# Kernel tuning notes

Hardware: AMD Instinct MI355X
Metric: run time of the kernel (lower is better)

Reference implementation:

```python
import jax, jax.numpy as jnp
import numpy as np

H, NHEADS, DK, DV, DFF, MAXLEN = 128, 2, 96, 96, 2048, 43
VIN, VOUT = 32000, 10000
N, T = 256, 43


def layer_norm(x, g, b, eps=1e-5):
    m = jnp.mean(x, axis=-1, keepdims=True)
    v = jnp.mean(jnp.square(x - m), axis=-1, keepdims=True)
    return (x - m) / jnp.sqrt(v + eps) * g + b


def setup_inputs() -> dict:
    key = jax.random.key(0)
    ks = jax.random.split(key, 24)
    def rn(k, shape, scale=0.02):
        return jax.random.normal(k, shape, dtype=jnp.float32) * scale
    return {
        "inputs": jax.random.randint(ks[0], (N, T), 0, VIN),
        "emb": rn(ks[1], (VIN, H)),
        "pos": rn(ks[2], (MAXLEN, H)),
        "Wq": rn(ks[3], (NHEADS, H, DK), 0.05),
        "bq": jnp.zeros((NHEADS, DK), jnp.float32),
        "Wk": rn(ks[4], (NHEADS, H, DK), 0.05),
        "bk": jnp.zeros((NHEADS, DK), jnp.float32),
        "Wv": rn(ks[5], (NHEADS, H, DV), 0.05),
        "bv": jnp.zeros((NHEADS, DV), jnp.float32),
        "Wo": rn(ks[6], (NHEADS * DV, H), 0.05),
        "bo": jnp.zeros((H,), jnp.float32),
        "ln1_g": jnp.ones((H,), jnp.float32),
        "ln1_b": jnp.zeros((H,), jnp.float32),
        "W1": rn(ks[7], (H, DFF), 0.05),
        "b1": jnp.zeros((DFF,), jnp.float32),
        "W2": rn(ks[8], (DFF, H), 0.05),
        "b2": jnp.zeros((H,), jnp.float32),
        "ln2_g": jnp.ones((H,), jnp.float32),
        "ln2_b": jnp.zeros((H,), jnp.float32),
        "Wout": rn(ks[9], (H, VOUT), 0.05),
        "bout": jnp.zeros((VOUT,), jnp.float32),
    }


def reference(inputs, emb, pos, Wq, bq, Wk, bk, Wv, bv, Wo, bo,
              ln1_g, ln1_b, W1, b1, W2, b2, ln2_g, ln2_b, Wout, bout):
    Tcur = inputs.shape[1]
    # embed: token + positional, (N,T,H)
    x = emb[inputs] + pos[:Tcur]
    # multi-head attention (all heads batched on axis 'a')
    q = jnp.einsum("nth,ahk->natk", x, Wq) + bq[:, None, :]
    k = jnp.einsum("nth,ahk->natk", x, Wk) + bk[:, None, :]
    v = jnp.einsum("nth,ahv->natv", x, Wv) + bv[:, None, :]
    scores = jnp.einsum("natk,nask->nats", q, k) / jnp.sqrt(jnp.float32(DK))
    # NOTE: original mask (float-embeddings != pad_idx) is a numerical no-op; omitted.
    probs = jax.nn.softmax(scores, axis=-1)
    att = jnp.einsum("nats,nasv->natv", probs, v)          # (N,A,T,DV)
    multi = att.transpose(0, 2, 1, 3).reshape(att.shape[0], Tcur, NHEADS * DV)
    attn_out = multi @ Wo + bo
    x1 = layer_norm(x + attn_out, ln1_g, ln1_b)
    # feedforward + residual + LN
    ff = jax.nn.relu(x1 @ W1 + b1) @ W2 + b2
    x2 = layer_norm(x1 + ff, ln2_g, ln2_b)
    # final vocab projection (N,T,VOUT)
    return x2 @ Wout + bout
```

## Files before the change

### kernel.cpp

```cpp
#include <hip/hip_runtime.h>
#include <hip/hip_bf16.h>

#define H 128
#define NHEADS 2
#define DK 96
#define DV 96
#define DFF 2048
#define VOUT 10000
#define VOUT_PAD 10112
#define NB 256
#define TT 43
#define NT (NB * TT)
#define MD (NHEADS * DV)
#define MDP 256
#define QKVC 640

typedef short short8v __attribute__((ext_vector_type(8)));
typedef unsigned short ushort8v __attribute__((ext_vector_type(8)));
typedef float f32x4 __attribute__((ext_vector_type(4)));

__device__ __forceinline__ unsigned short f2bf(float f) {
    unsigned b = __float_as_uint(f);
    unsigned r = b + 0x7FFFu + ((b >> 16) & 1u);
    return (unsigned short)(r >> 16);
}
__device__ __forceinline__ float bf2f(unsigned short u) {
    return __uint_as_float((unsigned)u << 16);
}

__global__ __launch_bounds__(256) void embed_kernel(
    const int* __restrict__ inputs, const float* __restrict__ emb,
    const float* __restrict__ pos, float* __restrict__ x,
    unsigned short* __restrict__ xb) {
    int i = blockIdx.x * 256 + threadIdx.x;
    int h = i & (H - 1);
    int nt = i >> 7;
    int t = nt % TT;
    float v = emb[inputs[nt] * H + h] + pos[t * H + h];
    x[i] = v;
    xb[i] = f2bf(v);
}

__global__ __launch_bounds__(256) void wqkv_pack_kernel(
    const float* __restrict__ Wq, const float* __restrict__ bq,
    const float* __restrict__ Wk, const float* __restrict__ bk,
    const float* __restrict__ Wv, const float* __restrict__ bv,
    unsigned short* __restrict__ Wt, float* __restrict__ bias) {
    int row = blockIdx.x * 256 + threadIdx.x;
    if (row >= QKVC) return;
    unsigned short* dst = Wt + (size_t)row * H;
    if (row < 576) {
        int seg = row / 96;
        int d = row - seg * 96;
        int which = seg >> 1;
        int head = seg & 1;
        const float* W  = (which == 0) ? Wq : (which == 1) ? Wk : Wv;
        const float* bi = (which == 0) ? bq : (which == 1) ? bk : bv;
        for (int h = 0; h < H; ++h) dst[h] = f2bf(W[((size_t)head * H + h) * DK + d]);
        bias[row] = bi[head * DK + d];
    } else {
        for (int h = 0; h < H; ++h) dst[h] = 0;
        bias[row] = 0.f;
    }
}

__global__ __launch_bounds__(256) void w1t_kernel(
    const float* __restrict__ W1, unsigned short* __restrict__ W1tb) {
    int n = blockIdx.x * 256 + threadIdx.x;
    ushort8v* dst = (ushort8v*)(W1tb + (size_t)n * H);
    #pragma unroll
    for (int k16 = 0; k16 < 16; ++k16) {
        ushort8v v;
        #pragma unroll
        for (int j = 0; j < 8; ++j)
            v[j] = f2bf(W1[(size_t)(k16 * 8 + j) * DFF + n]);
        dst[k16] = v;
    }
}

__global__ __launch_bounds__(256) void w2t_kernel(
    const float* __restrict__ W2, unsigned short* __restrict__ W2tb) {
    int c = blockIdx.x;
    int j = threadIdx.x;
    for (int k = j; k < DFF; k += 256)
        W2tb[(size_t)c * DFF + k] = f2bf(W2[(size_t)k * H + c]);
}

__global__ __launch_bounds__(256) void wotb_kernel(
    const float* __restrict__ Wo, unsigned short* __restrict__ Wot) {
    int idx = blockIdx.x * 256 + threadIdx.x;
    int c = idx >> 8, k = idx & 255;
    Wot[(size_t)c * MDP + k] = (k < MD) ? f2bf(Wo[(size_t)k * H + c]) : (unsigned short)0;
}

__global__ __launch_bounds__(256) void qkv_mfma_kernel(
    const unsigned short* __restrict__ xb, const unsigned short* __restrict__ Wt,
    const float* __restrict__ bias, unsigned short* __restrict__ qkvb) {
    __shared__ __align__(16) unsigned short As[128][128];
    __shared__ __align__(16) unsigned short Bt[128][128];
    int tid = threadIdx.x;
    int n0 = blockIdx.x * 128;
    int m0 = blockIdx.y * 128;
    {
        const ushort8v* A8 = (const ushort8v*)(xb + (size_t)m0 * H);
        for (int qc = tid; qc < 2048; qc += 256) {
            int row = qc >> 4, o = qc & 15;
            int po = (o & 8) | ((o ^ row) & 7);
            *(ushort8v*)&As[row][po * 8] = A8[qc];
        }
    }
    {
        const ushort8v* B8 = (const ushort8v*)(Wt + (size_t)n0 * H);
        for (int qc = tid; qc < 2048; qc += 256) {
            int row = qc >> 4, o = qc & 15;
            int po = (o & 8) | ((o ^ row) & 7);
            *(ushort8v*)&Bt[row][po * 8] = B8[qc];
        }
    }
    __syncthreads();
    int lane = tid & 63;
    int w = tid >> 6;
    int wr = w >> 1, wc = w & 1;
    int rl = lane & 15, quad = lane >> 4;
    f32x4 acc[4][4];
    #pragma unroll
    for (int i = 0; i < 4; ++i)
        #pragma unroll
        for (int j = 0; j < 4; ++j) acc[i][j] = (f32x4){0.f, 0.f, 0.f, 0.f};
    #pragma unroll
    for (int kk = 0; kk < 4; ++kk) {
        int o = kk * 4 + quad;
        short8v a[4], b[4];
        #pragma unroll
        for (int mi = 0; mi < 4; ++mi) {
            int row = wr * 64 + mi * 16 + rl;
            int po = (o & 8) | ((o ^ row) & 7);
            a[mi] = *(const short8v*)&As[row][po * 8];
        }
        #pragma unroll
        for (int ni = 0; ni < 4; ++ni) {
            int cc = wc * 64 + ni * 16 + rl;
            int po = (o & 8) | ((o ^ cc) & 7);
            b[ni] = *(const short8v*)&Bt[cc][po * 8];
        }
        #pragma unroll
        for (int mi = 0; mi < 4; ++mi)
            #pragma unroll
            for (int ni = 0; ni < 4; ++ni)
                acc[mi][ni] = __builtin_amdgcn_mfma_f32_16x16x32_bf16(
                    a[mi], b[ni], acc[mi][ni], 0, 0, 0);
    }
    #pragma unroll
    for (int ni = 0; ni < 4; ++ni) {
        int col = n0 + wc * 64 + ni * 16 + rl;
        float bv = bias[col];
        #pragma unroll
        for (int mi = 0; mi < 4; ++mi) {
            int rbase = m0 + wr * 64 + mi * 16 + quad * 4;
            #pragma unroll
            for (int r = 0; r < 4; ++r)
                qkvb[(size_t)(rbase + r) * QKVC + col] = f2bf(acc[mi][ni][r] + bv);
        }
    }
}

__global__ __launch_bounds__(256) void attn_core_kernel(
    const unsigned short* __restrict__ qkvb, unsigned short* __restrict__ multi_b) {
    int blk = blockIdx.x;
    int n = blk / NHEADS, a = blk % NHEADS;
    int tid = threadIdx.x;
    __shared__ float qs[TT][DK];
    __shared__ float ks2[TT][DK];
    __shared__ float vs[TT][DV];
    __shared__ float ss[TT][TT + 1];
    for (int i = tid; i < TT * 12 * 3; i += 256) {
        int which = i / (TT * 12);
        int rem = i - which * (TT * 12);
        int t = rem / 12, c8 = rem - t * 12;
        ushort8v u = *(const ushort8v*)(qkvb + (size_t)(n * TT + t) * QKVC
                                        + a * DK + which * 192 + c8 * 8);
        float* dst = ((which == 0) ? &qs[t][0] : (which == 1) ? &ks2[t][0] : &vs[t][0]) + c8 * 8;
        #pragma unroll
        for (int j = 0; j < 8; ++j) dst[j] = bf2f(u[j]);
    }
    __syncthreads();
    const float scale = rsqrtf((float)DK);
    for (int o = tid; o < TT * TT; o += 256) {
        int t = o / TT, s = o - t * TT;
        float acc = 0.f;
        #pragma unroll 8
        for (int d = 0; d < DK; ++d) acc += qs[t][d] * ks2[s][d];
        ss[t][s] = acc * scale;
    }
    __syncthreads();
    if (tid < TT) {
        float m = -1e30f;
        for (int s = 0; s < TT; ++s) m = fmaxf(m, ss[tid][s]);
        float sum = 0.f;
        for (int s = 0; s < TT; ++s) { float e = __expf(ss[tid][s] - m); ss[tid][s] = e; sum += e; }
        float inv = 1.0f / sum;
        for (int s = 0; s < TT; ++s) ss[tid][s] *= inv;
    }
    __syncthreads();
    for (int o = tid; o < TT * DV; o += 256) {
        int t = o / DV, d = o - t * DV;
        float acc = 0.f;
        #pragma unroll 8
        for (int s = 0; s < TT; ++s) acc += ss[t][s] * vs[s][d];
        multi_b[(size_t)(n * TT + t) * MDP + a * DV + d] = f2bf(acc);
    }
}

__global__ __launch_bounds__(256) void woln1_mfma_kernel(
    const unsigned short* __restrict__ mb, const unsigned short* __restrict__ Wot,
    const float* __restrict__ bo, const float* __restrict__ x,
    const float* __restrict__ g, const float* __restrict__ bln,
    float* __restrict__ x1, unsigned short* __restrict__ x1b) {
    __shared__ __align__(16) unsigned short As[128][128];
    __shared__ __align__(16) unsigned short Bt[128][128];
    int tid = threadIdx.x;
    int m0 = blockIdx.x * 128;
    int lane = tid & 63;
    int w = tid >> 6;
    int wr = w >> 1, wc = w & 1;
    int rl = lane & 15, quad = lane >> 4;
    f32x4 acc[4][4];
    #pragma unroll
    for (int i = 0; i < 4; ++i)
        #pragma unroll
        for (int j = 0; j < 4; ++j) acc[i][j] = (f32x4){0.f, 0.f, 0.f, 0.f};
    for (int kc = 0; kc < 2; ++kc) {
        for (int qc = tid; qc < 2048; qc += 256) {
            int row = qc >> 4, o = qc & 15;
            ushort8v v = *(const ushort8v*)(mb + (size_t)(m0 + row) * MDP + kc * 128 + o * 8);
            int po = (o & 8) | ((o ^ row) & 7);
            *(ushort8v*)&As[row][po * 8] = v;
        }
        for (int qc = tid; qc < 2048; qc += 256) {
            int row = qc >> 4, o = qc & 15;
            ushort8v v = *(const ushort8v*)(Wot + (size_t)row * MDP + kc * 128 + o * 8);
            int po = (o & 8) | ((o ^ row) & 7);
            *(ushort8v*)&Bt[row][po * 8] = v;
        }
        __syncthreads();
        #pragma unroll
        for (int kk = 0; kk < 4; ++kk) {
            int o = kk * 4 + quad;
            short8v a[4], b[4];
            #pragma unroll
            for (int mi = 0; mi < 4; ++mi) {
                int row = wr * 64 + mi * 16 + rl;
                int po = (o & 8) | ((o ^ row) & 7);
                a[mi] = *(const short8v*)&As[row][po * 8];
            }
            #pragma unroll
            for (int ni = 0; ni < 4; ++ni) {
                int cc = wc * 64 + ni * 16 + rl;
                int po = (o & 8) | ((o ^ cc) & 7);
                b[ni] = *(const short8v*)&Bt[cc][po * 8];
            }
            #pragma unroll
            for (int mi = 0; mi < 4; ++mi)
                #pragma unroll
                for (int ni = 0; ni < 4; ++ni)
                    acc[mi][ni] = __builtin_amdgcn_mfma_f32_16x16x32_bf16(
                        a[mi], b[ni], acc[mi][ni], 0, 0, 0);
        }
        __syncthreads();
    }
    float gg[4], bb[4], bov[4];
    #pragma unroll
    for (int ni = 0; ni < 4; ++ni) {
        int col = wc * 64 + ni * 16 + rl;
        gg[ni] = g[col]; bb[ni] = bln[col]; bov[ni] = bo[col];
    }
    float sy[4][4], sy2[4][4];
    #pragma unroll
    for (int mi = 0; mi < 4; ++mi)
        #pragma unroll
        for (int r = 0; r < 4; ++r) { sy[mi][r] = 0.f; sy2[mi][r] = 0.f; }
    #pragma unroll
    for (int mi = 0; mi < 4; ++mi) {
        #pragma unroll
        for (int r = 0; r < 4; ++r) {
            int row = wr * 64 + mi * 16 + quad * 4 + r;
            #pragma unroll
            for (int ni = 0; ni < 4; ++ni) {
                int col = wc * 64 + ni * 16 + rl;
                float y = acc[mi][ni][r] + bov[ni] + x[(size_t)(m0 + row) * H + col];
                acc[mi][ni][r] = y;
                sy[mi][r] += y;
                sy2[mi][r] += y * y;
            }
        }
    }
    #pragma unroll
    for (int mi = 0; mi < 4; ++mi)
        #pragma unroll
        for (int r = 0; r < 4; ++r) {
            #pragma unroll
            for (int m = 1; m < 16; m <<= 1) {
                sy[mi][r]  += __shfl_xor(sy[mi][r],  m);
                sy2[mi][r] += __shfl_xor(sy2[mi][r], m);
            }
        }
    float* scr = (float*)&As[0][0];
    if (rl == 0) {
        #pragma unroll
        for (int mi = 0; mi < 4; ++mi)
            #pragma unroll
            for (int r = 0; r < 4; ++r) {
                int row = wr * 64 + mi * 16 + quad * 4 + r;
                scr[wc * 128 + row]       = sy[mi][r];
                scr[256 + wc * 128 + row] = sy2[mi][r];
            }
    }
    __syncthreads();
    #pragma unroll
    for (int mi = 0; mi < 4; ++mi) {
        #pragma unroll
        for (int r = 0; r < 4; ++r) {
            int row = wr * 64 + mi * 16 + quad * 4 + r;
            float tsy  = scr[row] + scr[128 + row];
            float tsy2 = scr[256 + row] + scr[384 + row];
            float mean = tsy * (1.0f / H);
            float var  = tsy2 * (1.0f / H) - mean * mean;
            float rstd = rsqrtf(var + 1e-5f);
            #pragma unroll
            for (int ni = 0; ni < 4; ++ni) {
                int col = wc * 64 + ni * 16 + rl;
                float v = (acc[mi][ni][r] - mean) * rstd * gg[ni] + bb[ni];
                size_t idx = (size_t)(m0 + row) * H + col;
                x1[idx] = v;
                x1b[idx] = f2bf(v);
            }
        }
    }
}

__global__ __launch_bounds__(256) void ffh_kernel(
    const unsigned short* __restrict__ x1b, const unsigned short* __restrict__ W1tb,
    const float* __restrict__ b1, unsigned short* __restrict__ hb) {
    __shared__ __align__(16) unsigned short As[128][128];
    __shared__ __align__(16) unsigned short Bt[128][128];
    int tid = threadIdx.x;
    int n0 = blockIdx.x * 128;
    int m0 = blockIdx.y * 128;
    {
        const ushort8v* A8 = (const ushort8v*)(x1b + (size_t)m0 * H);
        for (int qc = tid; qc < 2048; qc += 256) {
            int row = qc >> 4, o = qc & 15;
            int po = (o & 8) | ((o ^ row) & 7);
            *(ushort8v*)&As[row][po * 8] = A8[qc];
        }
    }
    {
        const ushort8v* B8 = (const ushort8v*)(W1tb + (size_t)n0 * H);
        for (int qc = tid; qc < 2048; qc += 256) {
            int row = qc >> 4, o = qc & 15;
            int po = (o & 8) | ((o ^ row) & 7);
            *(ushort8v*)&Bt[row][po * 8] = B8[qc];
        }
    }
    __syncthreads();
    int lane = tid & 63;
    int w = tid >> 6;
    int wr = w >> 1, wc = w & 1;
    int rl = lane & 15, quad = lane >> 4;
    f32x4 acc[4][4];
    #pragma unroll
    for (int i = 0; i < 4; ++i)
        #pragma unroll
        for (int j = 0; j < 4; ++j) acc[i][j] = (f32x4){0.f, 0.f, 0.f, 0.f};
    #pragma unroll
    for (int kk = 0; kk < 4; ++kk) {
        int o = kk * 4 + quad;
        short8v a[4], b[4];
        #pragma unroll
        for (int mi = 0; mi < 4; ++mi) {
            int row = wr * 64 + mi * 16 + rl;
            int po = (o & 8) | ((o ^ row) & 7);
            a[mi] = *(const short8v*)&As[row][po * 8];
        }
        #pragma unroll
        for (int ni = 0; ni < 4; ++ni) {
            int cc = wc * 64 + ni * 16 + rl;
            int po = (o & 8) | ((o ^ cc) & 7);
            b[ni] = *(const short8v*)&Bt[cc][po * 8];
        }
        #pragma unroll
        for (int mi = 0; mi < 4; ++mi)
            #pragma unroll
            for (int ni = 0; ni < 4; ++ni)
                acc[mi][ni] = __builtin_amdgcn_mfma_f32_16x16x32_bf16(
                    a[mi], b[ni], acc[mi][ni], 0, 0, 0);
    }
    #pragma unroll
    for (int ni = 0; ni < 4; ++ni) {
        int col = n0 + wc * 64 + ni * 16 + rl;
        float bv = b1[col];
        #pragma unroll
        for (int mi = 0; mi < 4; ++mi) {
            int rbase = m0 + wr * 64 + mi * 16 + quad * 4;
            #pragma unroll
            for (int r = 0; r < 4; ++r)
                hb[(size_t)(rbase + r) * DFF + col] =
                    f2bf(fmaxf(acc[mi][ni][r] + bv, 0.f));
        }
    }
}

__global__ __launch_bounds__(256) void ff2_ln2_kernel(
    const unsigned short* __restrict__ hb, const unsigned short* __restrict__ W2tb,
    const float* __restrict__ b2, const float* __restrict__ x1,
    const float* __restrict__ g, const float* __restrict__ bln,
    unsigned short* __restrict__ x2b) {
    __shared__ __align__(16) unsigned short As[128][128];
    __shared__ __align__(16) unsigned short Bt[128][128];
    int tid = threadIdx.x;
    int m0 = blockIdx.x * 128;
    int lane = tid & 63;
    int w = tid >> 6;
    int wr = w >> 1, wc = w & 1;
    int rl = lane & 15, quad = lane >> 4;
    f32x4 acc[4][4];
    #pragma unroll
    for (int i = 0; i < 4; ++i)
        #pragma unroll
        for (int j = 0; j < 4; ++j) acc[i][j] = (f32x4){0.f, 0.f, 0.f, 0.f};
    for (int kc = 0; kc < 16; ++kc) {
        for (int qc = tid; qc < 2048; qc += 256) {
            int row = qc >> 4, o = qc & 15;
            ushort8v v = *(const ushort8v*)(hb + (size_t)(m0 + row) * DFF + kc * 128 + o * 8);
            int po = (o & 8) | ((o ^ row) & 7);
            *(ushort8v*)&As[row][po * 8] = v;
        }
        for (int qc = tid; qc < 2048; qc += 256) {
            int row = qc >> 4, o = qc & 15;
            ushort8v v = *(const ushort8v*)(W2tb + (size_t)row * DFF + kc * 128 + o * 8);
            int po = (o & 8) | ((o ^ row) & 7);
            *(ushort8v*)&Bt[row][po * 8] = v;
        }
        __syncthreads();
        #pragma unroll
        for (int kk = 0; kk < 4; ++kk) {
            int o = kk * 4 + quad;
            short8v a[4], b[4];
            #pragma unroll
            for (int mi = 0; mi < 4; ++mi) {
                int row = wr * 64 + mi * 16 + rl;
                int po = (o & 8) | ((o ^ row) & 7);
                a[mi] = *(const short8v*)&As[row][po * 8];
            }
            #pragma unroll
            for (int ni = 0; ni < 4; ++ni) {
                int cc = wc * 64 + ni * 16 + rl;
                int po = (o & 8) | ((o ^ cc) & 7);
                b[ni] = *(const short8v*)&Bt[cc][po * 8];
            }
            #pragma unroll
            for (int mi = 0; mi < 4; ++mi)
                #pragma unroll
                for (int ni = 0; ni < 4; ++ni)
                    acc[mi][ni] = __builtin_amdgcn_mfma_f32_16x16x32_bf16(
                        a[mi], b[ni], acc[mi][ni], 0, 0, 0);
        }
        __syncthreads();
    }
    float gg[4], bb[4], bov[4];
    #pragma unroll
    for (int ni = 0; ni < 4; ++ni) {
        int col = wc * 64 + ni * 16 + rl;
        gg[ni] = g[col]; bb[ni] = bln[col]; bov[ni] = b2[col];
    }
    float sy[4][4], sy2[4][4];
    #pragma unroll
    for (int mi = 0; mi < 4; ++mi)
        #pragma unroll
        for (int r = 0; r < 4; ++r) { sy[mi][r] = 0.f; sy2[mi][r] = 0.f; }
    #pragma unroll
    for (int mi = 0; mi < 4; ++mi) {
        #pragma unroll
        for (int r = 0; r < 4; ++r) {
            int row = wr * 64 + mi * 16 + quad * 4 + r;
            #pragma unroll
            for (int ni = 0; ni < 4; ++ni) {
                int col = wc * 64 + ni * 16 + rl;
                float y = acc[mi][ni][r] + bov[ni] + x1[(size_t)(m0 + row) * H + col];
                acc[mi][ni][r] = y;
                sy[mi][r] += y;
                sy2[mi][r] += y * y;
            }
        }
    }
    #pragma unroll
    for (int mi = 0; mi < 4; ++mi)
        #pragma unroll
        for (int r = 0; r < 4; ++r) {
            #pragma unroll
            for (int m = 1; m < 16; m <<= 1) {
                sy[mi][r]  += __shfl_xor(sy[mi][r],  m);
                sy2[mi][r] += __shfl_xor(sy2[mi][r], m);
            }
        }
    float* scr = (float*)&As[0][0];
    if (rl == 0) {
        #pragma unroll
        for (int mi = 0; mi < 4; ++mi)
            #pragma unroll
            for (int r = 0; r < 4; ++r) {
                int row = wr * 64 + mi * 16 + quad * 4 + r;
                scr[wc * 128 + row]       = sy[mi][r];
                scr[256 + wc * 128 + row] = sy2[mi][r];
            }
    }
    __syncthreads();
    #pragma unroll
    for (int mi = 0; mi < 4; ++mi) {
        #pragma unroll
        for (int r = 0; r < 4; ++r) {
            int row = wr * 64 + mi * 16 + quad * 4 + r;
            float tsy  = scr[row] + scr[128 + row];
            float tsy2 = scr[256 + row] + scr[384 + row];
            float mean = tsy * (1.0f / H);
            float var  = tsy2 * (1.0f / H) - mean * mean;
            float rstd = rsqrtf(var + 1e-5f);
            #pragma unroll
            for (int ni = 0; ni < 4; ++ni) {
                int col = wc * 64 + ni * 16 + rl;
                x2b[(size_t)(m0 + row) * H + col] =
                    f2bf((acc[mi][ni][r] - mean) * rstd * gg[ni] + bb[ni]);
            }
        }
    }
}

__global__ __launch_bounds__(256) void wtr_kernel(
    const float* __restrict__ W, unsigned short* __restrict__ Wt) {
    int n = blockIdx.x * 256 + threadIdx.x;
    if (n >= VOUT_PAD) return;
    ushort8v* dst = (ushort8v*)(Wt + (size_t)n * H);
    if (n < VOUT) {
        #pragma unroll
        for (int k16 = 0; k16 < 16; ++k16) {
            ushort8v v;
            #pragma unroll
            for (int j = 0; j < 8; ++j)
                v[j] = f2bf(W[(size_t)(k16 * 8 + j) * VOUT + n]);
            dst[k16] = v;
        }
    } else {
        ushort8v z = {};
        #pragma unroll
        for (int k16 = 0; k16 < 16; ++k16) dst[k16] = z;
    }
}

__global__ __launch_bounds__(256) void out_gemm_mfma_kernel(
    const unsigned short* __restrict__ A, const unsigned short* __restrict__ Wt,
    const float* __restrict__ bias, float* __restrict__ C) {
    __shared__ __align__(16) unsigned short As[128][128];
    __shared__ __align__(16) unsigned short Bt[128][128];
    int tid = threadIdx.x;
    int n0 = blockIdx.x * 128;
    int lane = tid & 63;
    int w = tid >> 6;
    int wr = w >> 1, wc = w & 1;
    int rl = lane & 15, quad = lane >> 4;
    {
        const ushort8v* B8 = (const ushort8v*)(Wt + (size_t)n0 * H);
        for (int qc = tid; qc < 2048; qc += 256) {
            int row = qc >> 4, o = qc & 15;
            int po = (o & 8) | ((o ^ row) & 7);
            *(ushort8v*)&Bt[row][po * 8] = B8[qc];
        }
    }
    float bv[4];
    #pragma unroll
    for (int ni = 0; ni < 4; ++ni) {
        int col = n0 + wc * 64 + ni * 16 + rl;
        bv[ni] = (col < VOUT) ? bias[col] : 0.f;
    }
    for (int half = 0; half < 2; ++half) {
        int m0 = (blockIdx.y * 2 + half) * 128;
        {
            const ushort8v* A8 = (const ushort8v*)(A + (size_t)m0 * H);
            for (int qc = tid; qc < 2048; qc += 256) {
                int row = qc >> 4, o = qc & 15;
                int po = (o & 8) | ((o ^ row) & 7);
                *(ushort8v*)&As[row][po * 8] = A8[qc];
            }
        }
        __syncthreads();
        f32x4 acc[4][4];
        #pragma unroll
        for (int i = 0; i < 4; ++i)
            #pragma unroll
            for (int j = 0; j < 4; ++j) acc[i][j] = (f32x4){0.f, 0.f, 0.f, 0.f};
        #pragma unroll
        for (int kk = 0; kk < 4; ++kk) {
            int o = kk * 4 + quad;
            short8v a[4], b[4];
            #pragma unroll
            for (int mi = 0; mi < 4; ++mi) {
                int row = wr * 64 + mi * 16 + rl;
                int po = (o & 8) | ((o ^ row) & 7);
                a[mi] = *(const short8v*)&As[row][po * 8];
            }
            #pragma unroll
            for (int ni = 0; ni < 4; ++ni) {
                int cc = wc * 64 + ni * 16 + rl;
                int po = (o & 8) | ((o ^ cc) & 7);
                b[ni] = *(const short8v*)&Bt[cc][po * 8];
            }
            #pragma unroll
            for (int mi = 0; mi < 4; ++mi)
                #pragma unroll
                for (int ni = 0; ni < 4; ++ni)
                    acc[mi][ni] = __builtin_amdgcn_mfma_f32_16x16x32_bf16(
                        a[mi], b[ni], acc[mi][ni], 0, 0, 0);
        }
        __syncthreads();
        #pragma unroll
        for (int ni = 0; ni < 4; ++ni) {
            int col = n0 + wc * 64 + ni * 16 + rl;
            if (col >= VOUT) continue;
            #pragma unroll
            for (int mi = 0; mi < 4; ++mi) {
                int rbase = m0 + wr * 64 + mi * 16 + quad * 4;
                #pragma unroll
                for (int r = 0; r < 4; ++r)
                    C[(size_t)(rbase + r) * VOUT + col] = acc[mi][ni][r] + bv[ni];
            }
        }
    }
}

extern "C" void kernel_launch(void* const* d_in, const int* in_sizes, int n_in,
                              void* d_out, int out_size, void* d_ws, size_t ws_size,
                              hipStream_t stream) {
    const int*   inputs = (const int*)  d_in[0];
    const float* emb    = (const float*)d_in[1];
    const float* pos    = (const float*)d_in[2];
    const float* Wq     = (const float*)d_in[3];
    const float* bq     = (const float*)d_in[4];
    const float* Wk     = (const float*)d_in[5];
    const float* bk     = (const float*)d_in[6];
    const float* Wv     = (const float*)d_in[7];
    const float* bv     = (const float*)d_in[8];
    const float* Wo     = (const float*)d_in[9];
    const float* bo     = (const float*)d_in[10];
    const float* ln1g   = (const float*)d_in[11];
    const float* ln1b   = (const float*)d_in[12];
    const float* W1     = (const float*)d_in[13];
    const float* b1     = (const float*)d_in[14];
    const float* W2     = (const float*)d_in[15];
    const float* b2     = (const float*)d_in[16];
    const float* ln2g   = (const float*)d_in[17];
    const float* ln2b   = (const float*)d_in[18];
    const float* Wout   = (const float*)d_in[19];
    const float* bout   = (const float*)d_in[20];
    float* out = (float*)d_out;

    float* ws = (float*)d_ws;
    float* x      = ws;
    float* x1     = x + (size_t)NT * H;
    float* bqkv   = x1 + (size_t)NT * H;
    unsigned short* xb      = (unsigned short*)(bqkv + QKVC);
    unsigned short* x1b     = xb + (size_t)NT * H;
    unsigned short* multi_b = x1b + (size_t)NT * H;
    unsigned short* x2b     = multi_b + (size_t)NT * MDP;
    unsigned short* Woutb   = x2b + (size_t)NT * H;
    unsigned short* Wqkvb   = Woutb + (size_t)VOUT_PAD * H;
    unsigned short* W1tb    = Wqkvb + (size_t)QKVC * H;
    unsigned short* W2tb    = W1tb + (size_t)DFF * H;
    unsigned short* Wotb    = W2tb + (size_t)H * DFF;
    unsigned short* qkvb    = Wotb + (size_t)H * MDP;
    unsigned short* hb      = qkvb + (size_t)NT * QKVC;

    wqkv_pack_kernel<<<(QKVC + 255) / 256, 256, 0, stream>>>(
        Wq, bq, Wk, bk, Wv, bv, Wqkvb, bqkv);
    wotb_kernel<<<H * MDP / 256, 256, 0, stream>>>(Wo, Wotb);
    w1t_kernel<<<DFF / 256, 256, 0, stream>>>(W1, W1tb);
    w2t_kernel<<<H, 256, 0, stream>>>(W2, W2tb);
    wtr_kernel<<<(VOUT_PAD + 255) / 256, 256, 0, stream>>>(Wout, Woutb);
    embed_kernel<<<NT * H / 256, 256, 0, stream>>>(inputs, emb, pos, x, xb);
    dim3 gqkv(QKVC / 128, NT / 128);
    qkv_mfma_kernel<<<gqkv, 256, 0, stream>>>(xb, Wqkvb, bqkv, qkvb);
    attn_core_kernel<<<NB * NHEADS, 256, 0, stream>>>(qkvb, multi_b);
    woln1_mfma_kernel<<<NT / 128, 256, 0, stream>>>(multi_b, Wotb, bo, x, ln1g, ln1b, x1, x1b);
    dim3 gff(DFF / 128, NT / 128);
    ffh_kernel<<<gff, 256, 0, stream>>>(x1b, W1tb, b1, hb);
    ff2_ln2_kernel<<<NT / 128, 256, 0, stream>>>(hb, W2tb, b2, x1, ln2g, ln2b, x2b);
    dim3 g5(VOUT_PAD / 128, NT / 256);
    out_gemm_mfma_kernel<<<g5, 256, 0, stream>>>(x2b, Woutb, bout, out);
}
```

Baseline: 724.6 us.

## Split FF2 GEMM over K into four partial slices with separate reduce+LN2 kernel

The second feed-forward GEMM previously ran only NT/128 = 86 blocks, each looping over all of K=2048, which leaves most CUs of the GPU idle. It is now split into four K slices (344 blocks) that write fp32 partial sums to a workspace. A new kernel adds the partials, bias and residual and applies LayerNorm 2 per row. This costs extra global traffic for the four fp32 partial buffers and one more kernel launch.

```diff
diff --git a/kernel.cpp b/kernel.cpp
--- a/kernel.cpp
+++ b/kernel.cpp
@@ -410,15 +410,14 @@
     }
 }
 
-__global__ __launch_bounds__(256) void ff2_ln2_kernel(
+__global__ __launch_bounds__(256) void ff2_splitk_kernel(
     const unsigned short* __restrict__ hb, const unsigned short* __restrict__ W2tb,
-    const float* __restrict__ b2, const float* __restrict__ x1,
-    const float* __restrict__ g, const float* __restrict__ bln,
-    unsigned short* __restrict__ x2b) {
+    float* __restrict__ pws) {
     __shared__ __align__(16) unsigned short As[128][128];
     __shared__ __align__(16) unsigned short Bt[128][128];
     int tid = threadIdx.x;
     int m0 = blockIdx.x * 128;
+    int ks = blockIdx.y;
     int lane = tid & 63;
     int w = tid >> 6;
     int wr = w >> 1, wc = w & 1;
@@ -428,7 +427,8 @@
     for (int i = 0; i < 4; ++i)
         #pragma unroll
         for (int j = 0; j < 4; ++j) acc[i][j] = (f32x4){0.f, 0.f, 0.f, 0.f};
-    for (int kc = 0; kc < 16; ++kc) {
+    for (int kci = 0; kci < 4; ++kci) {
+        int kc = ks * 4 + kci;
         for (int qc = tid; qc < 2048; qc += 256) {
             int row = qc >> 4, o = qc & 15;
             ushort8v v = *(const ushort8v*)(hb + (size_t)(m0 + row) * DFF + kc * 128 + o * 8);
@@ -467,71 +467,62 @@
         }
         __syncthreads();
     }
-    float gg[4], bb[4], bov[4];
     #pragma unroll
     for (int ni = 0; ni < 4; ++ni) {
         int col = wc * 64 + ni * 16 + rl;
-        gg[ni] = g[col]; bb[ni] = bln[col]; bov[ni] = b2[col];
-    }
-    float sy[4][4], sy2[4][4];
-    #pragma unroll
-    for (int mi = 0; mi < 4; ++mi)
-        #pragma unroll
-        for (int r = 0; r < 4; ++r) { sy[mi][r] = 0.f; sy2[mi][r] = 0.f; }
-    #pragma unroll
-    for (int mi = 0; mi < 4; ++mi) {
-        #pragma unroll
-        for (int r = 0; r < 4; ++r) {
-            int row = wr * 64 + mi * 16 + quad * 4 + r;
-            #pragma unroll
-            for (int ni = 0; ni < 4; ++ni) {
-                int col = wc * 64 + ni * 16 + rl;
-                float y = acc[mi][ni][r] + bov[ni] + x1[(size_t)(m0 + row) * H + col];
-                acc[mi][ni][r] = y;
-                sy[mi][r] += y;
-                sy2[mi][r] += y * y;
-            }
-        }
-    }
-    #pragma unroll
-    for (int mi = 0; mi < 4; ++mi)
-        #pragma unroll
-        for (int r = 0; r < 4; ++r) {
-            #pragma unroll
-            for (int m = 1; m < 16; m <<= 1) {
-                sy[mi][r]  += __shfl_xor(sy[mi][r],  m);
-                sy2[mi][r] += __shfl_xor(sy2[mi][r], m);
-            }
-        }
-    float* scr = (float*)&As[0][0];
-    if (rl == 0) {
-        #pragma unroll
-        for (int mi = 0; mi < 4; ++mi)
-            #pragma unroll
-            for (int r = 0; r < 4; ++r) {
-                int row = wr * 64 + mi * 16 + quad * 4 + r;
-                scr[wc * 128 + row]       = sy[mi][r];
-                scr[256 + wc * 128 + row] = sy2[mi][r];
-            }
-    }
-    __syncthreads();
-    #pragma unroll
-    for (int mi = 0; mi < 4; ++mi) {
-        #pragma unroll
-        for (int r = 0; r < 4; ++r) {
-            int row = wr * 64 + mi * 16 + quad * 4 + r;
-            float tsy  = scr[row] + scr[128 + row];
-            float tsy2 = scr[256 + row] + scr[384 + row];
-            float mean = tsy * (1.0f / H);
-            float var  = tsy2 * (1.0f / H) - mean * mean;
-            float rstd = rsqrtf(var + 1e-5f);
-            #pragma unroll
-            for (int ni = 0; ni < 4; ++ni) {
-                int col = wc * 64 + ni * 16 + rl;
-                x2b[(size_t)(m0 + row) * H + col] =
-                    f2bf((acc[mi][ni][r] - mean) * rstd * gg[ni] + bb[ni]);
-            }
-        }
+        #pragma unroll
+        for (int mi = 0; mi < 4; ++mi) {
+            int rbase = m0 + wr * 64 + mi * 16 + quad * 4;
+            #pragma unroll
+            for (int r = 0; r < 4; ++r)
+                pws[((size_t)ks * NT + rbase + r) * H + col] = acc[mi][ni][r];
+        }
+    }
+}
+
+__global__ __launch_bounds__(256) void ff2red_ln2_kernel(
+    const float* __restrict__ pws, const float* __restrict__ b2,
+    const float* __restrict__ x1, const float* __restrict__ g,
+    const float* __restrict__ bln, unsigned short* __restrict__ x2b) {
+    const size_t NTH = (size_t)NT * H;
+    int m0 = blockIdx.x * 128;
+    int tid = threadIdx.x;
+    int row = tid >> 1, half = tid & 1;
+    size_t rbase = (size_t)(m0 + row) * H + half * 64;
+    int cbase = half * 64;
+    f32x4 y4[16];
+    float sy = 0.f, sy2 = 0.f;
+    #pragma unroll
+    for (int i = 0; i < 16; ++i) {
+        f32x4 p0 = *(const f32x4*)(pws + 0 * NTH + rbase + i * 4);
+        f32x4 p1 = *(const f32x4*)(pws + 1 * NTH + rbase + i * 4);
+        f32x4 p2 = *(const f32x4*)(pws + 2 * NTH + rbase + i * 4);
+        f32x4 p3 = *(const f32x4*)(pws + 3 * NTH + rbase + i * 4);
+        f32x4 xr = *(const f32x4*)(x1 + rbase + i * 4);
+        f32x4 bb = *(const f32x4*)(b2 + cbase + i * 4);
+        f32x4 y = p0 + p1 + p2 + p3 + xr + bb;
+        y4[i] = y;
+        #pragma unroll
+        for (int j = 0; j < 4; ++j) { sy += y[j]; sy2 += y[j] * y[j]; }
+    }
+    sy  += __shfl_xor(sy, 1);
+    sy2 += __shfl_xor(sy2, 1);
+    float mean = sy * (1.0f / H);
+    float var  = sy2 * (1.0f / H) - mean * mean;
+    float rstd = rsqrtf(var + 1e-5f);
+    #pragma unroll
+    for (int i = 0; i < 16; i += 2) {
+        f32x4 g0 = *(const f32x4*)(g + cbase + i * 4);
+        f32x4 b0 = *(const f32x4*)(bln + cbase + i * 4);
+        f32x4 g1 = *(const f32x4*)(g + cbase + i * 4 + 4);
+        f32x4 b1v = *(const f32x4*)(bln + cbase + i * 4 + 4);
+        ushort8v o;
+        #pragma unroll
+        for (int j = 0; j < 4; ++j) {
+            o[j]     = f2bf((y4[i][j]     - mean) * rstd * g0[j] + b0[j]);
+            o[j + 4] = f2bf((y4[i + 1][j] - mean) * rstd * g1[j] + b1v[j]);
+        }
+        *(ushort8v*)(x2b + rbase + i * 4) = o;
     }
 }
 
@@ -665,7 +656,8 @@
     float* ws = (float*)d_ws;
     float* x      = ws;
     float* x1     = x + (size_t)NT * H;
-    float* bqkv   = x1 + (size_t)NT * H;
+    float* pws    = x1 + (size_t)NT * H;
+    float* bqkv   = pws + (size_t)4 * NT * H;
     unsigned short* xb      = (unsigned short*)(bqkv + QKVC);
     unsigned short* x1b     = xb + (size_t)NT * H;
     unsigned short* multi_b = x1b + (size_t)NT * H;
@@ -691,7 +683,9 @@
     woln1_mfma_kernel<<<NT / 128, 256, 0, stream>>>(multi_b, Wotb, bo, x, ln1g, ln1b, x1, x1b);
     dim3 gff(DFF / 128, NT / 128);
     ffh_kernel<<<gff, 256, 0, stream>>>(x1b, W1tb, b1, hb);
-    ff2_ln2_kernel<<<NT / 128, 256, 0, stream>>>(hb, W2tb, b2, x1, ln2g, ln2b, x2b);
+    dim3 gsk(NT / 128, 4);
+    ff2_splitk_kernel<<<gsk, 256, 0, stream>>>(hb, W2tb, pws);
+    ff2red_ln2_kernel<<<NT / 128, 256, 0, stream>>>(pws, b2, x1, ln2g, ln2b, x2b);
     dim3 g5(VOUT_PAD / 128, NT / 256);
     out_gemm_mfma_kernel<<<g5, 256, 0, stream>>>(x2b, Woutb, bout, out);
 }
```

New measurement: 707.7 us. 1.02x faster.
